# Kernel optimization log

Measured on AMD Instinct MI355X. Metric: run time of the kernel, lower is better.

Reference implementation:

```python
import jax, jax.numpy as jnp
import numpy as np

N_NODES = 50000
N_EDGES = 400000
V = 3        # view_num
D = 128      # per-view input width (nfeat / view_num)
H = 128      # nhid


def setup_inputs() -> dict:
    key = jax.random.key(0)
    k_h, k_src, k_dst, k_w1, k_w2 = jax.random.split(key, 5)
    h = jax.random.normal(k_h, (N_NODES, V * D), dtype=jnp.float32)
    src = jax.random.randint(k_src, (N_EDGES,), 0, N_NODES, dtype=jnp.int32)
    dst = jax.random.randint(k_dst, (N_EDGES,), 0, N_NODES, dtype=jnp.int32)
    s1 = 1.0 / np.sqrt(D)
    s2 = 1.0 / np.sqrt(H)
    W1 = jax.random.uniform(k_w1, (V, D, H), dtype=jnp.float32, minval=-s1, maxval=s1)
    b1 = jnp.zeros((V, H), dtype=jnp.float32)
    W2 = jax.random.uniform(k_w2, (H, H), dtype=jnp.float32, minval=-s2, maxval=s2)
    b2 = jnp.zeros((H,), dtype=jnp.float32)
    return {"h": h, "src": src, "dst": dst, "W1": W1, "b1": b1, "W2": W2, "b2": b2}


def _agg(x, src, dst, n_nodes):
    # DGL GraphConv(norm='none') aggregation: out[d] = sum_{(s->d) in E} x[s]
    return jax.ops.segment_sum(x[src], dst, num_segments=n_nodes)


def reference(h, src, dst, W1, b1, W2, b2):
    n = h.shape[0]
    x = h.reshape(n, V, D)  # split into views along feature dim
    # layer 1 (per-view GraphConv + relu):  relu( A @ (x_v W1_v) + b1_v )
    xw = jnp.einsum('nvd,vdh->nvh', x, W1)
    y = jax.nn.relu(_agg(xw, src, dst, n) + b1)
    # dropout p=0 / eval mode -> identity
    # layer 2 (shared GraphConv + relu)
    yw = jnp.einsum('nvh,hk->nvk', y, W2)
    z = jax.nn.relu(_agg(yw, src, dst, n) + b2)
    # agg_type=0 -> plain concat of views
    return z.reshape(n, V * H)
```

## Files before the change

kernel.cpp:

```cpp
#include <hip/hip_runtime.h>

constexpr int NN = 50000;
constexpr int NE = 400000;
constexpr int NV = 3;
constexpr int DF = 128;
constexpr int F  = 384;
constexpr int TR = 32;
constexpr int NB = (NN + 255) / 256;
constexpr int SP = 136;

typedef short  bf16x8 __attribute__((ext_vector_type(8)));
typedef float  f32x4  __attribute__((ext_vector_type(4)));


__device__ __forceinline__ ushort f2bf(float f) {
  unsigned u = __float_as_uint(f);
  u = (u + 0x7fffu + ((u >> 16) & 1u)) >> 16;
  return (ushort)u;
}


__device__ __forceinline__ void wprep_one(const float* __restrict__ W,
                                          ushort* __restrict__ pk, int idx) {
  int j = idx & 7, lane = (idx >> 3) & 63, cb = (idx >> 9) & 7, kb = (idx >> 12) & 3;
  int vs = idx >> 14;
  int v = vs >> 1, s = vs & 1;
  int d = kb * 32 + (lane >> 4) * 8 + j;
  int c = cb * 16 + (lane & 15);
  float w = W[((size_t)v * DF + d) * DF + c];
  ushort hi = f2bf(w);
  ushort outv = hi;
  if (s) outv = f2bf(w - __uint_as_float((unsigned)hi << 16));
  pk[idx] = outv;
}

constexpr int WB1 = (NV * 2 * 16384) / 256;
constexpr int WB2 = (2 * 16384) / 256;

__global__ void k_prep0(const float* __restrict__ W1, const float* __restrict__ W2,
                        ushort* __restrict__ w1pk, ushort* __restrict__ w2pk,
                        int* __restrict__ deg) {
  int b = blockIdx.x, t = threadIdx.x;
  if (b < WB1) {
    wprep_one(W1, w1pk, b * 256 + t);
  } else if (b < WB1 + WB2) {
    wprep_one(W2, w2pk, (b - WB1) * 256 + t);
  } else {
    int i = (b - WB1 - WB2) * 256 + t;
    if (i < NN) deg[i] = 0;
  }
}


__global__ void k_cvtcnt(const float* __restrict__ in, ushort* __restrict__ outb,
                         const int* __restrict__ dst, int* __restrict__ deg) {
  int b = blockIdx.x, t = threadIdx.x;
  if (b < 2048) {
    const int n4 = NN * F / 4;
    const float4* in4 = (const float4*)in;
    for (int k = b * 256 + t; k < n4; k += 2048 * 256) {
      float4 x = in4[k];
      ushort4 u;
      u.x = f2bf(x.x); u.y = f2bf(x.y); u.z = f2bf(x.z); u.w = f2bf(x.w);
      *(ushort4*)(outb + (size_t)k * 4) = u;
    }
  } else {
    for (int e = (b - 2048) * 256 + t; e < NE; e += 1024 * 256)
      atomicAdd(&deg[dst[e]], 1);
  }
}


__global__ void k_blocksum(const int* __restrict__ deg, int* __restrict__ bsum) {
  __shared__ int s[4];
  int i = blockIdx.x * 256 + threadIdx.x;
  int v = (i < NN) ? deg[i] : 0;
  for (int o = 32; o > 0; o >>= 1) v += __shfl_down(v, o);
  if ((threadIdx.x & 63) == 0) s[threadIdx.x >> 6] = v;
  __syncthreads();
  if (threadIdx.x == 0) bsum[blockIdx.x] = s[0] + s[1] + s[2] + s[3];
}

__global__ void k_scanpar(int* __restrict__ bsum, int* __restrict__ offs_n) {
  __shared__ int s[256];
  int t = threadIdx.x;
  int v = (t < NB) ? bsum[t] : 0;
  s[t] = v;
  __syncthreads();
  for (int o = 1; o < 256; o <<= 1) {
    int add = (t >= o) ? s[t - o] : 0;
    __syncthreads();
    s[t] += add;
    __syncthreads();
  }
  if (t < NB) bsum[t] = s[t] - v;
  if (t == NB - 1) *offs_n = s[t];
}

__global__ void k_offsets(const int* __restrict__ deg, const int* __restrict__ bsum,
                          int* __restrict__ offs) {
  __shared__ int s[256];
  int t = threadIdx.x;
  int i = blockIdx.x * 256 + t;
  int v = (i < NN) ? deg[i] : 0;
  s[t] = v;
  __syncthreads();
  for (int o = 1; o < 256; o <<= 1) {
    int add = (t >= o) ? s[t - o] : 0;
    __syncthreads();
    s[t] += add;
    __syncthreads();
  }
  if (i < NN) offs[i] = bsum[blockIdx.x] + s[t] - v;
}

__global__ void k_scatter(const int* __restrict__ src, const int* __restrict__ dst,
                          const int* __restrict__ offs, int* __restrict__ deg,
                          int* __restrict__ csr) {
  int i = blockIdx.x * blockDim.x + threadIdx.x;
  int stride = gridDim.x * blockDim.x;
  for (int e = i; e < NE; e += stride) {
    int d = dst[e];
    int pos = offs[d] + atomicSub(&deg[d], 1) - 1;
    csr[pos] = src[e];
  }
}


template <bool OUT_BF16>
__global__ __launch_bounds__(256, 4)
void k_layer(const ushort* __restrict__ feat,
             const int* __restrict__ offs, const int* __restrict__ csr,
             const ushort* __restrict__ Wpk, int vmul,
             const float* __restrict__ ball, int bstride,
             void* __restrict__ outp) {
  __shared__ ushort sThi[TR][SP];
  __shared__ ushort sTlo[TR][SP];
  const int t = threadIdx.x;
  const int v = blockIdx.y;
  const float* __restrict__ bias = ball + (size_t)v * bstride;

  const int wave = t >> 6, lane = t & 63;
  const int lane15 = lane & 15, lgrp = lane >> 4;
  const int row0 = blockIdx.x * TR;
  const int vcol = v * DF + lane * 2;
  const int lane2 = lane * 2;

#pragma unroll
  for (int rr = 0; rr < TR / 4; ++rr) {
    int r = rr * 4 + wave;
    int node = row0 + r;
    float ax = 0.f, ay = 0.f;
    if (node < NN) {
      int e0 = offs[node], e1 = offs[node + 1];
      int e = e0;
      while (e < e1) {
        int n = e1 - e; if (n > 64) n = 64;
        int ce = e + lane; if (ce > e1 - 1) ce = e1 - 1;
        int idx = csr[ce];
        int j = 0;
        for (; j + 8 <= n; j += 8) {
          int s0 = __builtin_amdgcn_readlane(idx, j);
          int s1 = __builtin_amdgcn_readlane(idx, j + 1);
          int s2 = __builtin_amdgcn_readlane(idx, j + 2);
          int s3 = __builtin_amdgcn_readlane(idx, j + 3);
          int s4 = __builtin_amdgcn_readlane(idx, j + 4);
          int s5 = __builtin_amdgcn_readlane(idx, j + 5);
          int s6 = __builtin_amdgcn_readlane(idx, j + 6);
          int s7 = __builtin_amdgcn_readlane(idx, j + 7);
          unsigned u0 = *(const unsigned*)(feat + (size_t)s0 * F + vcol);
          unsigned u1 = *(const unsigned*)(feat + (size_t)s1 * F + vcol);
          unsigned u2 = *(const unsigned*)(feat + (size_t)s2 * F + vcol);
          unsigned u3 = *(const unsigned*)(feat + (size_t)s3 * F + vcol);
          unsigned u4 = *(const unsigned*)(feat + (size_t)s4 * F + vcol);
          unsigned u5 = *(const unsigned*)(feat + (size_t)s5 * F + vcol);
          unsigned u6 = *(const unsigned*)(feat + (size_t)s6 * F + vcol);
          unsigned u7 = *(const unsigned*)(feat + (size_t)s7 * F + vcol);
          ax += __uint_as_float(u0 << 16); ay += __uint_as_float(u0 & 0xffff0000u);
          ax += __uint_as_float(u1 << 16); ay += __uint_as_float(u1 & 0xffff0000u);
          ax += __uint_as_float(u2 << 16); ay += __uint_as_float(u2 & 0xffff0000u);
          ax += __uint_as_float(u3 << 16); ay += __uint_as_float(u3 & 0xffff0000u);
          ax += __uint_as_float(u4 << 16); ay += __uint_as_float(u4 & 0xffff0000u);
          ax += __uint_as_float(u5 << 16); ay += __uint_as_float(u5 & 0xffff0000u);
          ax += __uint_as_float(u6 << 16); ay += __uint_as_float(u6 & 0xffff0000u);
          ax += __uint_as_float(u7 << 16); ay += __uint_as_float(u7 & 0xffff0000u);
        }
        if (j + 4 <= n) {
          int s0 = __builtin_amdgcn_readlane(idx, j);
          int s1 = __builtin_amdgcn_readlane(idx, j + 1);
          int s2 = __builtin_amdgcn_readlane(idx, j + 2);
          int s3 = __builtin_amdgcn_readlane(idx, j + 3);
          unsigned u0 = *(const unsigned*)(feat + (size_t)s0 * F + vcol);
          unsigned u1 = *(const unsigned*)(feat + (size_t)s1 * F + vcol);
          unsigned u2 = *(const unsigned*)(feat + (size_t)s2 * F + vcol);
          unsigned u3 = *(const unsigned*)(feat + (size_t)s3 * F + vcol);
          ax += __uint_as_float(u0 << 16); ay += __uint_as_float(u0 & 0xffff0000u);
          ax += __uint_as_float(u1 << 16); ay += __uint_as_float(u1 & 0xffff0000u);
          ax += __uint_as_float(u2 << 16); ay += __uint_as_float(u2 & 0xffff0000u);
          ax += __uint_as_float(u3 << 16); ay += __uint_as_float(u3 & 0xffff0000u);
          j += 4;
        }
        for (; j < n; ++j) {
          int s0 = __builtin_amdgcn_readlane(idx, j);
          unsigned u0 = *(const unsigned*)(feat + (size_t)s0 * F + vcol);
          ax += __uint_as_float(u0 << 16); ay += __uint_as_float(u0 & 0xffff0000u);
        }
        e += n;
      }
    }
    ushort hx = f2bf(ax);
    ushort lx = f2bf(ax - __uint_as_float((unsigned)hx << 16));
    ushort hy = f2bf(ay);
    ushort ly = f2bf(ay - __uint_as_float((unsigned)hy << 16));
    *(unsigned*)&sThi[r][lane2] = (unsigned)hx | ((unsigned)hy << 16);
    *(unsigned*)&sTlo[r][lane2] = (unsigned)lx | ((unsigned)ly << 16);
  }
  __syncthreads();

  const ushort* pkbase = Wpk + (size_t)(v * vmul) * (2 * 4 * 8 * 512);
  const float bv0 = bias[wave * 32 + lane15];
  const float bv1 = bias[wave * 32 + 16 + lane15];
  f32x4 acc00 = {bv0, bv0, bv0, bv0};
  f32x4 acc01 = {bv1, bv1, bv1, bv1};
  f32x4 acc10 = {bv0, bv0, bv0, bv0};
  f32x4 acc11 = {bv1, bv1, bv1, bv1};

#pragma unroll
  for (int kb = 0; kb < 4; ++kb) {
    const int acol = kb * 32 + lgrp * 8;
    bf16x8 ah0 = *(const bf16x8*)&sThi[lane15][acol];
    bf16x8 ah1 = *(const bf16x8*)&sThi[16 + lane15][acol];
    bf16x8 al0 = *(const bf16x8*)&sTlo[lane15][acol];
    bf16x8 al1 = *(const bf16x8*)&sTlo[16 + lane15][acol];
    bf16x8 bh0 = *(const bf16x8*)(pkbase + ((size_t)((0 * 4 + kb) * 8 + wave * 2 + 0)) * 512 + lane * 8);
    bf16x8 bh1 = *(const bf16x8*)(pkbase + ((size_t)((0 * 4 + kb) * 8 + wave * 2 + 1)) * 512 + lane * 8);
    bf16x8 bl0 = *(const bf16x8*)(pkbase + ((size_t)((1 * 4 + kb) * 8 + wave * 2 + 0)) * 512 + lane * 8);
    bf16x8 bl1 = *(const bf16x8*)(pkbase + ((size_t)((1 * 4 + kb) * 8 + wave * 2 + 1)) * 512 + lane * 8);
    acc00 = __builtin_amdgcn_mfma_f32_16x16x32_bf16(ah0, bh0, acc00, 0, 0, 0);
    acc00 = __builtin_amdgcn_mfma_f32_16x16x32_bf16(al0, bh0, acc00, 0, 0, 0);
    acc00 = __builtin_amdgcn_mfma_f32_16x16x32_bf16(ah0, bl0, acc00, 0, 0, 0);
    acc01 = __builtin_amdgcn_mfma_f32_16x16x32_bf16(ah0, bh1, acc01, 0, 0, 0);
    acc01 = __builtin_amdgcn_mfma_f32_16x16x32_bf16(al0, bh1, acc01, 0, 0, 0);
    acc01 = __builtin_amdgcn_mfma_f32_16x16x32_bf16(ah0, bl1, acc01, 0, 0, 0);
    acc10 = __builtin_amdgcn_mfma_f32_16x16x32_bf16(ah1, bh0, acc10, 0, 0, 0);
    acc10 = __builtin_amdgcn_mfma_f32_16x16x32_bf16(al1, bh0, acc10, 0, 0, 0);
    acc10 = __builtin_amdgcn_mfma_f32_16x16x32_bf16(ah1, bl0, acc10, 0, 0, 0);
    acc11 = __builtin_amdgcn_mfma_f32_16x16x32_bf16(ah1, bh1, acc11, 0, 0, 0);
    acc11 = __builtin_amdgcn_mfma_f32_16x16x32_bf16(al1, bh1, acc11, 0, 0, 0);
    acc11 = __builtin_amdgcn_mfma_f32_16x16x32_bf16(ah1, bl1, acc11, 0, 0, 0);
  }

  const int colbase = v * DF + wave * 32 + lane15;
#pragma unroll
  for (int rb = 0; rb < 2; ++rb) {
    f32x4 a0 = rb ? acc10 : acc00;
    f32x4 a1 = rb ? acc11 : acc01;
#pragma unroll
    for (int k = 0; k < 4; ++k) {
      int row = row0 + rb * 16 + lgrp * 4 + k;
      if (row < NN) {
        float x0 = a0[k] > 0.f ? a0[k] : 0.f;
        float x1 = a1[k] > 0.f ? a1[k] : 0.f;
        if (OUT_BF16) {
          ushort* ob = (ushort*)outp;
          ob[(size_t)row * F + colbase]      = f2bf(x0);
          ob[(size_t)row * F + colbase + 16] = f2bf(x1);
        } else {
          float* of = (float*)outp;
          of[(size_t)row * F + colbase]      = x0;
          of[(size_t)row * F + colbase + 16] = x1;
        }
      }
    }
  }
}


static inline size_t align_up(size_t x, size_t a) { return (x + a - 1) & ~(a - 1); }

extern "C" void kernel_launch(void* const* d_in, const int* in_sizes, int n_in,
                              void* d_out, int out_size, void* d_ws, size_t ws_size,
                              hipStream_t stream) {
  const float* h   = (const float*)d_in[0];
  const int*   src = (const int*)d_in[1];
  const int*   dst = (const int*)d_in[2];
  const float* W1  = (const float*)d_in[3];
  const float* b1  = (const float*)d_in[4];
  const float* W2  = (const float*)d_in[5];
  const float* b2  = (const float*)d_in[6];
  float* out = (float*)d_out;

  char* ws = (char*)d_ws;
  size_t o = 0;
  int* deg  = (int*)(ws + o); o = align_up(o + (size_t)NN * 4, 1024);
  int* offs = (int*)(ws + o); o = align_up(o + (size_t)(NN + 1) * 4, 1024);
  int* bsum = (int*)(ws + o); o = align_up(o + 1024, 1024);
  int* csr  = (int*)(ws + o); o = align_up(o + (size_t)NE * 4, 1024);
  ushort* hb   = (ushort*)(ws + o); o = align_up(o + (size_t)NN * F * 2, 1024);
  ushort* ybuf = (ushort*)(ws + o); o = align_up(o + (size_t)NN * F * 2, 1024);
  ushort* w1pk = (ushort*)(ws + o); o = align_up(o + (size_t)NV * 2 * 16384 * 2, 1024);
  ushort* w2pk = (ushort*)(ws + o); o = align_up(o + (size_t)1 * 2 * 16384 * 2, 1024);
  (void)ws_size; (void)n_in; (void)in_sizes; (void)out_size;

  k_prep0<<<WB1 + WB2 + NB, 256, 0, stream>>>(W1, W2, w1pk, w2pk, deg);
  k_cvtcnt<<<3072, 256, 0, stream>>>(h, hb, dst, deg);
  k_blocksum<<<NB, 256, 0, stream>>>(deg, bsum);
  k_scanpar<<<1, 256, 0, stream>>>(bsum, offs + NN);
  k_offsets<<<NB, 256, 0, stream>>>(deg, bsum, offs);
  k_scatter<<<1024, 256, 0, stream>>>(src, dst, offs, deg, csr);

  dim3 grid((NN + TR - 1) / TR, NV);
  k_layer<true ><<<grid, 256, 0, stream>>>(hb,   offs, csr, w1pk, 1, b1, DF, ybuf);
  k_layer<false><<<grid, 256, 0, stream>>>(ybuf, offs, csr, w2pk, 0, b2, 0,  out);
}
```

Before: 203.1 us.

## Process contiguous 8-row edge range per wave with shared CSR chunks

Each wave now handles 8 consecutive rows instead of interleaved rows, loading all 9 row offsets in one lane-parallel read and streaming the combined CSR edge range in 64-edge chunks shared across rows. This is meant to cut per-row offset loads and partially-filled CSR chunk loads for low-degree nodes, since the graph averages about 8 edges per node. In exchange it keeps 16 accumulators per lane, which raises register pressure, and the inner gather unroll drops from 8 to 4, which may reduce memory-level parallelism.

```diff
diff --git a/kernel.cpp b/kernel.cpp
--- a/kernel.cpp
+++ b/kernel.cpp
@@ -146,74 +146,65 @@
   const int vcol = v * DF + lane * 2;
   const int lane2 = lane * 2;
 
-#pragma unroll
-  for (int rr = 0; rr < TR / 4; ++rr) {
-    int r = rr * 4 + wave;
-    int node = row0 + r;
-    float ax = 0.f, ay = 0.f;
-    if (node < NN) {
-      int e0 = offs[node], e1 = offs[node + 1];
-      int e = e0;
-      while (e < e1) {
-        int n = e1 - e; if (n > 64) n = 64;
-        int ce = e + lane; if (ce > e1 - 1) ce = e1 - 1;
-        int idx = csr[ce];
-        int j = 0;
-        for (; j + 8 <= n; j += 8) {
-          int s0 = __builtin_amdgcn_readlane(idx, j);
-          int s1 = __builtin_amdgcn_readlane(idx, j + 1);
-          int s2 = __builtin_amdgcn_readlane(idx, j + 2);
-          int s3 = __builtin_amdgcn_readlane(idx, j + 3);
-          int s4 = __builtin_amdgcn_readlane(idx, j + 4);
-          int s5 = __builtin_amdgcn_readlane(idx, j + 5);
-          int s6 = __builtin_amdgcn_readlane(idx, j + 6);
-          int s7 = __builtin_amdgcn_readlane(idx, j + 7);
-          unsigned u0 = *(const unsigned*)(feat + (size_t)s0 * F + vcol);
-          unsigned u1 = *(const unsigned*)(feat + (size_t)s1 * F + vcol);
-          unsigned u2 = *(const unsigned*)(feat + (size_t)s2 * F + vcol);
-          unsigned u3 = *(const unsigned*)(feat + (size_t)s3 * F + vcol);
-          unsigned u4 = *(const unsigned*)(feat + (size_t)s4 * F + vcol);
-          unsigned u5 = *(const unsigned*)(feat + (size_t)s5 * F + vcol);
-          unsigned u6 = *(const unsigned*)(feat + (size_t)s6 * F + vcol);
-          unsigned u7 = *(const unsigned*)(feat + (size_t)s7 * F + vcol);
-          ax += __uint_as_float(u0 << 16); ay += __uint_as_float(u0 & 0xffff0000u);
-          ax += __uint_as_float(u1 << 16); ay += __uint_as_float(u1 & 0xffff0000u);
-          ax += __uint_as_float(u2 << 16); ay += __uint_as_float(u2 & 0xffff0000u);
-          ax += __uint_as_float(u3 << 16); ay += __uint_as_float(u3 & 0xffff0000u);
-          ax += __uint_as_float(u4 << 16); ay += __uint_as_float(u4 & 0xffff0000u);
-          ax += __uint_as_float(u5 << 16); ay += __uint_as_float(u5 & 0xffff0000u);
-          ax += __uint_as_float(u6 << 16); ay += __uint_as_float(u6 & 0xffff0000u);
-          ax += __uint_as_float(u7 << 16); ay += __uint_as_float(u7 & 0xffff0000u);
-        }
-        if (j + 4 <= n) {
-          int s0 = __builtin_amdgcn_readlane(idx, j);
-          int s1 = __builtin_amdgcn_readlane(idx, j + 1);
-          int s2 = __builtin_amdgcn_readlane(idx, j + 2);
-          int s3 = __builtin_amdgcn_readlane(idx, j + 3);
-          unsigned u0 = *(const unsigned*)(feat + (size_t)s0 * F + vcol);
-          unsigned u1 = *(const unsigned*)(feat + (size_t)s1 * F + vcol);
-          unsigned u2 = *(const unsigned*)(feat + (size_t)s2 * F + vcol);
-          unsigned u3 = *(const unsigned*)(feat + (size_t)s3 * F + vcol);
-          ax += __uint_as_float(u0 << 16); ay += __uint_as_float(u0 & 0xffff0000u);
-          ax += __uint_as_float(u1 << 16); ay += __uint_as_float(u1 & 0xffff0000u);
-          ax += __uint_as_float(u2 << 16); ay += __uint_as_float(u2 & 0xffff0000u);
-          ax += __uint_as_float(u3 << 16); ay += __uint_as_float(u3 & 0xffff0000u);
-          j += 4;
-        }
-        for (; j < n; ++j) {
-          int s0 = __builtin_amdgcn_readlane(idx, j);
-          unsigned u0 = *(const unsigned*)(feat + (size_t)s0 * F + vcol);
-          ax += __uint_as_float(u0 << 16); ay += __uint_as_float(u0 & 0xffff0000u);
-        }
-        e += n;
+  const int base = row0 + wave * 8;
+
+  int ow = 0;
+  {
+    int ri = base + lane;
+    if (lane <= 8) {
+      if (ri > NN) ri = NN;
+      ow = offs[ri];
+    }
+  }
+  int so[9];
+#pragma unroll
+  for (int k = 0; k < 9; ++k) so[k] = __builtin_amdgcn_readlane(ow, k);
+
+  float ax[8], ay[8];
+#pragma unroll
+  for (int r = 0; r < 8; ++r) { ax[r] = 0.f; ay[r] = 0.f; }
+
+  const int eb = so[0], ee = so[8];
+  for (int chunk = eb; chunk < ee; chunk += 64) {
+    int ce = chunk + lane; if (ce > ee - 1) ce = ee - 1;
+    int idx = csr[ce];
+    int cend = chunk + 64 < ee ? chunk + 64 : ee;
+#pragma unroll
+    for (int r = 0; r < 8; ++r) {
+      int js = so[r] > chunk ? so[r] : chunk;
+      int je = so[r + 1] < cend ? so[r + 1] : cend;
+      int j  = js - chunk;
+      int jn = je - chunk;
+      for (; j + 4 <= jn; j += 4) {
+        int s0 = __builtin_amdgcn_readlane(idx, j);
+        int s1 = __builtin_amdgcn_readlane(idx, j + 1);
+        int s2 = __builtin_amdgcn_readlane(idx, j + 2);
+        int s3 = __builtin_amdgcn_readlane(idx, j + 3);
+        unsigned u0 = *(const unsigned*)(feat + (size_t)s0 * F + vcol);
+        unsigned u1 = *(const unsigned*)(feat + (size_t)s1 * F + vcol);
+        unsigned u2 = *(const unsigned*)(feat + (size_t)s2 * F + vcol);
+        unsigned u3 = *(const unsigned*)(feat + (size_t)s3 * F + vcol);
+        ax[r] += __uint_as_float(u0 << 16); ay[r] += __uint_as_float(u0 & 0xffff0000u);
+        ax[r] += __uint_as_float(u1 << 16); ay[r] += __uint_as_float(u1 & 0xffff0000u);
+        ax[r] += __uint_as_float(u2 << 16); ay[r] += __uint_as_float(u2 & 0xffff0000u);
+        ax[r] += __uint_as_float(u3 << 16); ay[r] += __uint_as_float(u3 & 0xffff0000u);
+      }
+      for (; j < jn; ++j) {
+        int s0 = __builtin_amdgcn_readlane(idx, j);
+        unsigned u0 = *(const unsigned*)(feat + (size_t)s0 * F + vcol);
+        ax[r] += __uint_as_float(u0 << 16); ay[r] += __uint_as_float(u0 & 0xffff0000u);
       }
     }
-    ushort hx = f2bf(ax);
-    ushort lx = f2bf(ax - __uint_as_float((unsigned)hx << 16));
-    ushort hy = f2bf(ay);
-    ushort ly = f2bf(ay - __uint_as_float((unsigned)hy << 16));
-    *(unsigned*)&sThi[r][lane2] = (unsigned)hx | ((unsigned)hy << 16);
-    *(unsigned*)&sTlo[r][lane2] = (unsigned)lx | ((unsigned)ly << 16);
+  }
+
+#pragma unroll
+  for (int r = 0; r < 8; ++r) {
+    ushort hx = f2bf(ax[r]);
+    ushort lx = f2bf(ax[r] - __uint_as_float((unsigned)hx << 16));
+    ushort hy = f2bf(ay[r]);
+    ushort ly = f2bf(ay[r] - __uint_as_float((unsigned)hy << 16));
+    *(unsigned*)&sThi[wave * 8 + r][lane2] = (unsigned)hx | ((unsigned)hy << 16);
+    *(unsigned*)&sTlo[wave * 8 + r][lane2] = (unsigned)lx | ((unsigned)ly << 16);
   }
   __syncthreads();
 
```

Measured after the change: 196.1 us, median of 2. 1.04x faster.
